# Kernel tuning notes

Hardware: AMD Instinct MI355X
Metric: run time of the kernel (lower is better)

## Reference

```python
import jax, jax.numpy as jnp
import numpy as np


def _conv3x3(x, w):
    # NCHW input, OIHW weight, stride 1, padding 1 (SAME for 3x3)
    return jax.lax.conv_general_dilated(
        x, w, window_strides=(1, 1), padding=((1, 1), (1, 1)),
        dimension_numbers=('NCHW', 'OIHW', 'NCHW'))


def _conv1x1(x, w):
    return jax.lax.conv_general_dilated(
        x, w, window_strides=(1, 1), padding=((0, 0), (0, 0)),
        dimension_numbers=('NCHW', 'OIHW', 'NCHW'))


def setup_inputs() -> dict:
    key = jax.random.key(0)
    k_x, k_w1, k_w2, k_wm = jax.random.split(key, 4)
    N, C, H, W = 16, 256, 64, 64
    fan = C * 9
    x = jax.random.normal(k_x, (N, C, H, W), dtype=jnp.float32)
    w1 = jax.random.normal(k_w1, (C, C, 3, 3), dtype=jnp.float32) * (2.0 / fan) ** 0.5
    w2 = jax.random.normal(k_w2, (C, C, 3, 3), dtype=jnp.float32) * (2.0 / fan) ** 0.5
    w_mask = jax.random.normal(k_wm, (1, C, 1, 1), dtype=jnp.float32) * (1.0 / C) ** 0.5
    b_mask = jnp.zeros((1,), dtype=jnp.float32)
    return {'x': x, 'w1': w1, 'w2': w2, 'w_mask': w_mask, 'b_mask': b_mask}


def reference(x, w1, w2, w_mask, b_mask):
    # MaskUnit: 1x1 conv -> logits -> hard binary mask (straight-through estimator)
    logits = _conv1x1(x, w_mask) + b_mask[None, :, None, None]  # [N,1,H,W]
    hard = (logits > 0).astype(x.dtype)
    mask = logits + jax.lax.stop_gradient(hard - logits)        # std mask, binary in fwd
    # dilated mask: 3x3 max-pool (covers 3x3 receptive field of active outputs)
    mask_dilate = jax.lax.reduce_window(
        mask, -jnp.inf, jax.lax.max, (1, 1, 3, 3), (1, 1, 1, 1), 'SAME')
    # sparse branch: conv1 gated by dilated mask, conv2 gated by std mask
    h = jax.nn.relu(_conv3x3(x, w1) * mask_dilate)
    h = jax.nn.relu(_conv3x3(h, w2) * mask)
    # apply_mask + residual (mask binary -> h*mask == h already, kept for fidelity)
    out = x + h * mask
    return out
```

## Files before the change

kernel.cpp:

```cpp
#include <hip/hip_runtime.h>
#include <hip/hip_bf16.h>

#define C_ 256
#define H_ 64
#define W_ 64
#define N_ 16
#define HW_ 4096
#define IMG_ (C_ * HW_)
#define PADIMG_ (66 * 66 * 256)
#define WT_ELEMS_ (9 * 16 * 256 * 16)

typedef short bf16x8 __attribute__((ext_vector_type(8)));
typedef float f32x16 __attribute__((ext_vector_type(16)));

__device__ __forceinline__ unsigned short f2bf(float f) {
  __hip_bfloat16 h = __float2bfloat16(f);
  return *reinterpret_cast<unsigned short*>(&h);
}

__device__ __forceinline__ void gld_lds16(const void* g, void* l) {
  __builtin_amdgcn_global_load_lds(
      (const __attribute__((address_space(1))) void*)g,
      (__attribute__((address_space(3))) void*)l, 16, 0, 0);
}

__global__ __launch_bounds__(256) void xpadmask_kernel(
    const float* __restrict__ x, const float* __restrict__ wm,
    const float* __restrict__ bm, short* __restrict__ Xp,
    unsigned char* __restrict__ mask) {
  __shared__ unsigned short lds[64 * 260];
  __shared__ float wms[256];
  __shared__ double sums[4][64];
  const int h = blockIdx.x, img = blockIdx.y;
  const int tid = threadIdx.x;
  const int wv = tid >> 6, wl = tid & 63;
  wms[tid] = wm[tid];
  __syncthreads();
  const float* xi = x + (size_t)img * IMG_ + h * 64;
  double a0 = 0.0, a1 = 0.0, a2 = 0.0, a3 = 0.0;
#pragma unroll 4
  for (int i = 0; i < 16; ++i) {
#pragma unroll
    for (int u = 0; u < 4; ++u) {
      int c = (i * 4 + u) * 4 + wv;
      float v = xi[(size_t)c * HW_ + wl];
      lds[wl * 260 + c] = f2bf(v);
      double p = (double)v * (double)wms[c];
      if (u == 0) a0 += p;
      else if (u == 1) a1 += p;
      else if (u == 2) a2 += p;
      else a3 += p;
    }
  }
  sums[wv][wl] = (a0 + a1) + (a2 + a3);
  __syncthreads();
  short* Xpimg = Xp + (size_t)img * PADIMG_;
  short* Xpi = Xpimg + ((h + 1) * 66 + 1) * 256;
#pragma unroll
  for (int j = 0; j < 16; ++j) {
    int w = j * 4 + wv;
    int c4 = wl * 4;
    uint2 d = *(const uint2*)&lds[w * 260 + c4];
    *(uint2*)&Xpi[(size_t)w * 256 + c4] = d;
  }
  if (tid < 128) {
    const int side = tid >> 6;
    const int e = (tid & 63) * 4;
    *(uint2*)&Xpimg[((size_t)(h + 1) * 66 + side * 65) * 256 + e] =
        make_uint2(0u, 0u);
  }
  if (h == 0 || h == 63) {
    uint2* rowp = (uint2*)(Xpimg + (size_t)((h == 0) ? 0 : 65) * 66 * 256);
    for (int o = tid; o < 66 * 256 / 4; o += 256) rowp[o] = make_uint2(0u, 0u);
  }
  if (wv == 0) {
    double t = sums[0][wl] + sums[1][wl] + sums[2][wl] + sums[3][wl] +
               (double)bm[0];
    mask[img * HW_ + h * 64 + wl] = (t > 0.0) ? 1 : 0;
  }
}

__global__ __launch_bounds__(256) void wt_kernel(
    const float* __restrict__ w1, const float* __restrict__ w2,
    short* __restrict__ Wt1, short* __restrict__ Wt2) {
  const int k = blockIdx.x, c = threadIdx.x;
  const float* src = blockIdx.y ? w2 : w1;
  short* dst = blockIdx.y ? Wt2 : Wt1;
  const float* s = src + ((size_t)k * 256 + c) * 9;
  const int kc = c >> 4, ce = c & 15;
#pragma unroll
  for (int t = 0; t < 9; ++t)
    dst[(((size_t)t * 16 + kc) * 256 + k) * 16 + ce] = (short)f2bf(s[t]);
}

__global__ __launch_bounds__(128) void halo_zero(short* __restrict__ Hp) {
  int p = blockIdx.x;
  int r, c;
  if (p < 66) { r = 0; c = p; }
  else if (p < 132) { r = 65; c = p - 66; }
  else if (p < 196) { r = p - 131; c = 0; }
  else { r = p - 195; c = 65; }
  unsigned int* d = (unsigned int*)(Hp + (size_t)blockIdx.y * PADIMG_ +
                                    (size_t)(r * 66 + c) * 256);
  d[threadIdx.x] = 0u;
}

#define BBUF 10560
#define WOFF 21120
#define WBUF 9216

__device__ __forceinline__ void stage_BW(short* sm, int buf, const short* Xb,
                                         const short* Wg, int ch0, int kc,
                                         int wave, int lane) {
  short* Bd = sm + buf * BBUF;
  short* Wd = sm + WOFF + buf * WBUF;
  const int ko = kc * 16;
#pragma unroll
  for (int q = 0; q < 5; ++q) {
    const int n = wave + 8 * q;
    if (n < 22) {
      const int h = (n >= 11) ? 1 : 0;
      const int i = n - h * 11;
      const int row0 = (i < 10) ? i * 64 : 596;
      gld_lds16(Xb + (size_t)(row0 + lane) * 256 + ko + h * 8,
                Bd + h * 5280 + row0 * 8);
    } else {
      const int m = n - 22;
      const int t = m >> 1, ih = m & 1;
      gld_lds16(Wg + (((size_t)t * 16 + kc) * 256 + ch0 + ih * 32 +
                      (lane & 31)) * 16 + (lane >> 5) * 8,
                Wd + (t * 2 + ih) * 512);
    }
  }
}

template <int EPI>
__global__ __launch_bounds__(512, 4) void conv_mfma(
    const short* __restrict__ src, const short* __restrict__ Wt,
    const unsigned char* __restrict__ gate, const float* __restrict__ xres,
    short* __restrict__ dstH, float* __restrict__ dstF, int swz) {
  __shared__ __align__(16) short sm[2 * BBUF + 2 * WBUF];

  const int tid = threadIdx.x;
  const int lane = tid & 63, wave = tid >> 6;
  const int ln31 = lane & 31, kh = lane >> 5;

  int bx, by, bz;
  {
    int d = blockIdx.x + 4 * (blockIdx.y + 8 * blockIdx.z);
    if (swz) {
      int k = d & 7, j = d >> 3;
      bx = j & 3;
      by = (j >> 2) & 7;
      bz = ((j >> 5) << 3) + k;
    } else {
      bx = blockIdx.x;
      by = blockIdx.y;
      bz = blockIdx.z;
    }
  }
  const int ch0 = bx * 64;
  const int h0 = by * 8;
  const int img = bz;

  const short* Xb = src + (size_t)img * PADIMG_ + (size_t)(h0 * 66) * 256;

  f32x16 acc[2][2];
#pragma unroll
  for (int i = 0; i < 2; ++i)
#pragma unroll
    for (int j = 0; j < 2; ++j)
#pragma unroll
      for (int e = 0; e < 16; ++e) acc[i][j][e] = 0.f;

  stage_BW(sm, 0, Xb, Wt, ch0, 0, wave, lane);
  asm volatile("s_waitcnt vmcnt(0)\n\ts_barrier" ::: "memory");

  for (int kk = 0; kk < 16; ++kk) {
    const int cur = kk & 1;
    if (kk < 15) stage_BW(sm, cur ^ 1, Xb, Wt, ch0, kk + 1, wave, lane);

    const short* Bth = sm + cur * BBUF + kh * 5280 + (wave * 66 + ln31) * 8;
    const short* Wth = sm + WOFF + cur * WBUF + (kh * 32 + ln31) * 8;

    bf16x8 ac[2], bc[2], an[2], bn[2];
#pragma unroll
    for (int i = 0; i < 2; ++i)
      ac[i] = *(const bf16x8*)(Wth + (0 * 2 + i) * 512);
#pragma unroll
    for (int j = 0; j < 2; ++j)
      bc[j] = *(const bf16x8*)(Bth + (0 * 66 + j * 32 + 0) * 8);

#pragma unroll
    for (int t = 0; t < 9; ++t) {
      if (t == 3 || t == 6) asm volatile("s_barrier" ::: "memory");
      if (t < 8) {
        const int dy = (t + 1) / 3, dx = (t + 1) % 3;
#pragma unroll
        for (int i = 0; i < 2; ++i)
          an[i] = *(const bf16x8*)(Wth + ((t + 1) * 2 + i) * 512);
#pragma unroll
        for (int j = 0; j < 2; ++j)
          bn[j] = *(const bf16x8*)(Bth + (dy * 66 + j * 32 + dx) * 8);
      }
      if (t % 3 == 0) __builtin_amdgcn_s_setprio(1);
#pragma unroll
      for (int j = 0; j < 2; ++j) {
        acc[0][j] = __builtin_amdgcn_mfma_f32_32x32x16_bf16(ac[0], bc[j],
                                                            acc[0][j], 0, 0, 0);
        acc[1][j] = __builtin_amdgcn_mfma_f32_32x32x16_bf16(ac[1], bc[j],
                                                            acc[1][j], 0, 0, 0);
      }
      if (t % 3 == 2) __builtin_amdgcn_s_setprio(0);
      if (t < 8) {
#pragma unroll
        for (int i = 0; i < 2; ++i) ac[i] = an[i];
#pragma unroll
        for (int j = 0; j < 2; ++j) bc[j] = bn[j];
      }
    }
    if (kk < 15)
      asm volatile("s_waitcnt vmcnt(0)\n\ts_barrier" ::: "memory");
  }

  const int r = h0 + wave;
#pragma unroll
  for (int j = 0; j < 2; ++j) {
    const int col = j * 32 + ln31;
    const int pidx = r * 64 + col;
    unsigned int g;
    if (EPI == 0) {
      g = 0;
#pragma unroll
      for (int dy = -1; dy <= 1; ++dy) {
        const int rr = r + dy;
        if (rr < 0 || rr >= H_) continue;
#pragma unroll
        for (int dx = -1; dx <= 1; ++dx) {
          const int cc = col + dx;
          if (cc < 0 || cc >= W_) continue;
          g |= gate[img * HW_ + rr * W_ + cc];
        }
      }
    } else {
      g = gate[img * HW_ + pidx];
    }
#pragma unroll
    for (int i = 0; i < 2; ++i) {
      const f32x16 v = acc[i][j];
#pragma unroll
      for (int rg = 0; rg < 4; ++rg) {
        const int ch = ch0 + i * 32 + rg * 8 + kh * 4;
        float e0 = g ? fmaxf(v[rg * 4 + 0], 0.f) : 0.f;
        float e1 = g ? fmaxf(v[rg * 4 + 1], 0.f) : 0.f;
        float e2 = g ? fmaxf(v[rg * 4 + 2], 0.f) : 0.f;
        float e3 = g ? fmaxf(v[rg * 4 + 3], 0.f) : 0.f;
        if (EPI == 0) {
          uint2 u;
          u.x = (unsigned int)f2bf(e0) | ((unsigned int)f2bf(e1) << 16);
          u.y = (unsigned int)f2bf(e2) | ((unsigned int)f2bf(e3) << 16);
          short* dp = dstH + (size_t)img * PADIMG_ +
                      ((size_t)((r + 1) * 66 + (col + 1))) * 256 + ch;
          *(uint2*)dp = u;
        } else {
          size_t o = (size_t)img * IMG_ + (size_t)ch * HW_ + pidx;
          dstF[o] = xres[o] + e0;
          dstF[o + HW_] = xres[o + HW_] + e1;
          dstF[o + 2 * HW_] = xres[o + 2 * HW_] + e2;
          dstF[o + 3 * HW_] = xres[o + 3 * HW_] + e3;
        }
      }
    }
  }
}

extern "C" void kernel_launch(void* const* d_in, const int* in_sizes, int n_in,
                              void* d_out, int out_size, void* d_ws,
                              size_t ws_size, hipStream_t stream) {
  const float* x = (const float*)d_in[0];
  const float* w1 = (const float*)d_in[1];
  const float* w2 = (const float*)d_in[2];
  const float* wmask = (const float*)d_in[3];
  const float* bmask = (const float*)d_in[4];
  float* out = (float*)d_out;

  char* ws = (char*)d_ws;
  unsigned char* mask = (unsigned char*)ws;
  short* Wt1 = (short*)(ws + 65536);
  short* Wt2 = Wt1 + WT_ELEMS_;
  const size_t fixed = 65536 + 4 * (size_t)WT_ELEMS_;
  short* Xp = (short*)(ws + fixed);

  const size_t tailpad = 32768;
  const size_t per_img = 2 * (size_t)PADIMG_ * 2;
  int B = (ws_size > fixed + tailpad)
              ? (int)((ws_size - fixed - tailpad) / per_img) : 0;
  if (B > N_) B = N_;
  if (B < 1) B = 1;
  short* Hp = Xp + (size_t)B * PADIMG_;

  wt_kernel<<<dim3(256, 2), 256, 0, stream>>>(w1, w2, Wt1, Wt2);
  halo_zero<<<dim3(260, B), 128, 0, stream>>>(Hp);

  for (int n0 = 0; n0 < N_; n0 += B) {
    const int nb = (N_ - n0 < B) ? (N_ - n0) : B;
    const int swz = (nb % 8 == 0) ? 1 : 0;
    xpadmask_kernel<<<dim3(64, nb), 256, 0, stream>>>(
        x + (size_t)n0 * IMG_, wmask, bmask, Xp, mask + n0 * HW_);
    conv_mfma<0><<<dim3(4, 8, nb), 512, 0, stream>>>(
        Xp, Wt1, mask + n0 * HW_, nullptr, Hp, nullptr, swz);
    conv_mfma<1><<<dim3(4, 8, nb), 512, 0, stream>>>(
        Hp, Wt2, mask + n0 * HW_, x + (size_t)n0 * IMG_, nullptr,
        out + (size_t)n0 * IMG_, swz);
  }
}
```

Before: 288.5 us.

## Rotate tap order per wave and interleave staging loads into MFMA loop

Each wave now starts the 9-tap loop at a different tap, offset by its wave index, so waves read different LDS regions at the same time and bank or broadcast contention is spread out. The intra-iteration s_barriers at taps 3 and 6 are removed. The global-to-LDS staging of the next K-chunk is split into five single loads placed between the first MFMA steps instead of issued in one burst. This trades some address arithmetic for better overlap of memory issue with compute and fewer barriers.

```diff
diff --git a/kernel.cpp b/kernel.cpp
--- a/kernel.cpp
+++ b/kernel.cpp
@@ -109,28 +109,23 @@
 #define WOFF 21120
 #define WBUF 9216
 
-__device__ __forceinline__ void stage_BW(short* sm, int buf, const short* Xb,
-                                         const short* Wg, int ch0, int kc,
-                                         int wave, int lane) {
-  short* Bd = sm + buf * BBUF;
-  short* Wd = sm + WOFF + buf * WBUF;
+__device__ __forceinline__ void stage_one(short* sm, int buf, const short* Xb,
+                                          const short* Wg, int ch0, int kc,
+                                          int wave, int lane, int q) {
+  const int n = wave + 8 * q;
   const int ko = kc * 16;
-#pragma unroll
-  for (int q = 0; q < 5; ++q) {
-    const int n = wave + 8 * q;
-    if (n < 22) {
-      const int h = (n >= 11) ? 1 : 0;
-      const int i = n - h * 11;
-      const int row0 = (i < 10) ? i * 64 : 596;
-      gld_lds16(Xb + (size_t)(row0 + lane) * 256 + ko + h * 8,
-                Bd + h * 5280 + row0 * 8);
-    } else {
-      const int m = n - 22;
-      const int t = m >> 1, ih = m & 1;
-      gld_lds16(Wg + (((size_t)t * 16 + kc) * 256 + ch0 + ih * 32 +
-                      (lane & 31)) * 16 + (lane >> 5) * 8,
-                Wd + (t * 2 + ih) * 512);
-    }
+  if (n < 22) {
+    const int h = (n >= 11) ? 1 : 0;
+    const int i = n - h * 11;
+    const int row0 = (i < 10) ? i * 64 : 596;
+    gld_lds16(Xb + (size_t)(row0 + lane) * 256 + ko + h * 8,
+              sm + buf * BBUF + h * 5280 + row0 * 8);
+  } else {
+    const int m = n - 22;
+    const int t = m >> 1, ih = m & 1;
+    gld_lds16(Wg + (((size_t)t * 16 + kc) * 256 + ch0 + ih * 32 +
+                    (lane & 31)) * 16 + (lane >> 5) * 8,
+              sm + WOFF + buf * WBUF + (t * 2 + ih) * 512);
   }
 }
 
@@ -173,50 +168,53 @@
 #pragma unroll
       for (int e = 0; e < 16; ++e) acc[i][j][e] = 0.f;
 
-  stage_BW(sm, 0, Xb, Wt, ch0, 0, wave, lane);
+#pragma unroll
+  for (int q = 0; q < 5; ++q)
+    stage_one(sm, 0, Xb, Wt, ch0, 0, wave, lane, q);
   asm volatile("s_waitcnt vmcnt(0)\n\ts_barrier" ::: "memory");
 
   for (int kk = 0; kk < 16; ++kk) {
     const int cur = kk & 1;
-    if (kk < 15) stage_BW(sm, cur ^ 1, Xb, Wt, ch0, kk + 1, wave, lane);
-
     const short* Bth = sm + cur * BBUF + kh * 5280 + (wave * 66 + ln31) * 8;
     const short* Wth = sm + WOFF + cur * WBUF + (kh * 32 + ln31) * 8;
 
     bf16x8 ac[2], bc[2], an[2], bn[2];
-#pragma unroll
-    for (int i = 0; i < 2; ++i)
-      ac[i] = *(const bf16x8*)(Wth + (0 * 2 + i) * 512);
-#pragma unroll
-    for (int j = 0; j < 2; ++j)
-      bc[j] = *(const bf16x8*)(Bth + (0 * 66 + j * 32 + 0) * 8);
-
-#pragma unroll
-    for (int t = 0; t < 9; ++t) {
-      if (t == 3 || t == 6) asm volatile("s_barrier" ::: "memory");
-      if (t < 8) {
-        const int dy = (t + 1) / 3, dx = (t + 1) % 3;
-#pragma unroll
-        for (int i = 0; i < 2; ++i)
-          an[i] = *(const bf16x8*)(Wth + ((t + 1) * 2 + i) * 512);
-#pragma unroll
-        for (int j = 0; j < 2; ++j)
-          bn[j] = *(const bf16x8*)(Bth + (dy * 66 + j * 32 + dx) * 8);
+    {
+      const int tt = wave;
+      const int dy = (tt * 11) >> 5, dx = tt - 3 * dy;
+      const int bo = (dy * 66 + dx) * 8;
+      ac[0] = *(const bf16x8*)(Wth + tt * 1024);
+      ac[1] = *(const bf16x8*)(Wth + tt * 1024 + 512);
+      bc[0] = *(const bf16x8*)(Bth + bo);
+      bc[1] = *(const bf16x8*)(Bth + bo + 256);
+    }
+#pragma unroll
+    for (int u = 0; u < 9; ++u) {
+      if (u < 5 && kk < 15)
+        stage_one(sm, cur ^ 1, Xb, Wt, ch0, kk + 1, wave, lane, u);
+      if (u < 8) {
+        int tt = wave + u + 1;
+        if (tt >= 9) tt -= 9;
+        const int dy = (tt * 11) >> 5, dx = tt - 3 * dy;
+        const int bo = (dy * 66 + dx) * 8;
+        an[0] = *(const bf16x8*)(Wth + tt * 1024);
+        an[1] = *(const bf16x8*)(Wth + tt * 1024 + 512);
+        bn[0] = *(const bf16x8*)(Bth + bo);
+        bn[1] = *(const bf16x8*)(Bth + bo + 256);
       }
-      if (t % 3 == 0) __builtin_amdgcn_s_setprio(1);
-#pragma unroll
-      for (int j = 0; j < 2; ++j) {
-        acc[0][j] = __builtin_amdgcn_mfma_f32_32x32x16_bf16(ac[0], bc[j],
-                                                            acc[0][j], 0, 0, 0);
-        acc[1][j] = __builtin_amdgcn_mfma_f32_32x32x16_bf16(ac[1], bc[j],
-                                                            acc[1][j], 0, 0, 0);
-      }
-      if (t % 3 == 2) __builtin_amdgcn_s_setprio(0);
-      if (t < 8) {
-#pragma unroll
-        for (int i = 0; i < 2; ++i) ac[i] = an[i];
-#pragma unroll
-        for (int j = 0; j < 2; ++j) bc[j] = bn[j];
+      __builtin_amdgcn_s_setprio(1);
+      acc[0][0] = __builtin_amdgcn_mfma_f32_32x32x16_bf16(ac[0], bc[0],
+                                                          acc[0][0], 0, 0, 0);
+      acc[0][1] = __builtin_amdgcn_mfma_f32_32x32x16_bf16(ac[0], bc[1],
+                                                          acc[0][1], 0, 0, 0);
+      acc[1][0] = __builtin_amdgcn_mfma_f32_32x32x16_bf16(ac[1], bc[0],
+                                                          acc[1][0], 0, 0, 0);
+      acc[1][1] = __builtin_amdgcn_mfma_f32_32x32x16_bf16(ac[1], bc[1],
+                                                          acc[1][1], 0, 0, 0);
+      __builtin_amdgcn_s_setprio(0);
+      if (u < 8) {
+        ac[0] = an[0]; ac[1] = an[1];
+        bc[0] = bn[0]; bc[1] = bn[1];
       }
     }
     if (kk < 15)
```

Result: slower. 347.8 us (+20.6%).
